# Kernel tuning notes

Measured on AMD Instinct MI355X. Metric: run time of the kernel, lower is better.

The kernel has to match this reference:

```python
import jax, jax.numpy as jnp
import numpy as np


def setup_inputs() -> dict:
    key = jax.random.key(0)
    kx, ks = jax.random.split(key)
    M, N, D = 8192, 8192, 512
    X = jax.random.normal(kx, (M, D), dtype=jnp.float32)
    svs = jax.random.normal(ks, (N, D), dtype=jnp.float32)
    # scale = 1/(2*sigma^2); a plausible fitted value for standard-normal data
    scale = jnp.asarray(0.01, dtype=jnp.float32)
    return {"X": X, "svs": svs, "scale": scale}


def reference(X, svs, scale):
    N, D = svs.shape
    x2 = jnp.sum(X * X, axis=-1, keepdims=True)          # [M, 1]
    s2 = jnp.sum(svs * svs, axis=-1)                      # [N]
    dist2 = x2 + s2[None, :] - 2.0 * (X @ svs.T)          # [M, N]
    dist2 = jnp.maximum(dist2, 0.0)
    log_p = (jax.scipy.special.logsumexp(-scale * dist2, axis=-1)
             - jnp.log(jnp.asarray(N, dtype=X.dtype))
             + (D / 2) * jnp.log(scale / jnp.pi))
    return log_p
```

## Files before the change

kernel.cpp:

```cpp
#include <hip/hip_runtime.h>
#include <hip/hip_bf16.h>
#include <hip/hip_fp8.h>
#include <math.h>

typedef __attribute__((ext_vector_type(4))) int   int4v;
typedef __attribute__((ext_vector_type(8))) int   int8v;
typedef __attribute__((ext_vector_type(4))) float f32x4;

#define BM 128
#define BN 128
#define BK 128

union frag_u { int8v v; int4v h[2]; };

__global__ __launch_bounds__(256) void prep_kernel(
    const float* __restrict__ X, const float* __restrict__ S,
    unsigned char* __restrict__ Xq, unsigned char* __restrict__ Sq,
    float* __restrict__ x2, float* __restrict__ s2,
    float* __restrict__ rowsum, int M, int R, int Dv)
{
    const int gid  = blockIdx.x * 256 + threadIdx.x;
    const int nthr = gridDim.x * 256;

    for (int i = gid; i < M; i += nthr) rowsum[i] = 0.f;

    const int lane = threadIdx.x & 63;
    const int wid  = gid >> 6;
    const int nw   = nthr >> 6;

    for (int row = wid; row < R; row += nw) {
        const float* rp;
        unsigned char* op;
        float* sq;
        if (row < M) { rp = X + (size_t)row * Dv;       op = Xq + (size_t)row * Dv;       sq = x2 + row; }
        else         { rp = S + (size_t)(row - M) * Dv; op = Sq + (size_t)(row - M) * Dv; sq = s2 + (row - M); }

        float acc = 0.f;
        for (int k = lane * 8; k < Dv; k += 64 * 8) {
            float4 v0 = *(const float4*)(rp + k);
            float4 v1 = *(const float4*)(rp + k + 4);
            acc += v0.x * v0.x + v0.y * v0.y + v0.z * v0.z + v0.w * v0.w;
            acc += v1.x * v1.x + v1.y * v1.y + v1.z * v1.z + v1.w * v1.w;
            int lo = __builtin_amdgcn_cvt_pk_fp8_f32(v0.x, v0.y, 0, false);
            lo     = __builtin_amdgcn_cvt_pk_fp8_f32(v0.z, v0.w, lo, true);
            int hi = __builtin_amdgcn_cvt_pk_fp8_f32(v1.x, v1.y, 0, false);
            hi     = __builtin_amdgcn_cvt_pk_fp8_f32(v1.z, v1.w, hi, true);
            union { int i2[2]; uint2 u; } pk;
            pk.i2[0] = lo; pk.i2[1] = hi;
            *(uint2*)(op + k) = pk.u;
        }
#pragma unroll
        for (int off = 1; off < 64; off <<= 1)
            acc += __shfl_xor(acc, off, 64);
        if (lane == 0) *sq = acc;
    }
}

template<int DVC>
__global__ __launch_bounds__(256, 3) void kde_gemm_kernel(
    const unsigned char* __restrict__ Xq,
    const unsigned char* __restrict__ Sq,
    const float* __restrict__ x2,
    const float* __restrict__ s2,
    const float* __restrict__ scale_p,
    float* __restrict__ rowsum,
    int M, int N, int Dv)
{
    const int D = DVC ? DVC : Dv;

    __shared__ char smem[32768];
    unsigned char* As = (unsigned char*)smem;
    unsigned char* Bs = (unsigned char*)(smem + 16384);

    const int tid  = threadIdx.x;
    const int wave = tid >> 6;
    const int lane = tid & 63;
    const int quad = lane >> 4;
    const int l16  = lane & 15;

    const int m0 = blockIdx.x * BM;
    const int n0 = blockIdx.y * BN;
    const int wm = (wave & 1) * 64;
    const int wn = (wave >> 1) * 64;

    const float sc = *scale_p;

    f32x4 acc[4][4] = {};

    const int srow0 = wave * 8 + (lane >> 3);
    const int cg    = (lane & 7) ^ (lane >> 3);
    const unsigned char* gA = Xq + (size_t)(m0 + srow0) * D + cg * 16;
    const unsigned char* gB = Sq + (size_t)(n0 + srow0) * D + cg * 16;

    const int e     = l16 & 7;
    const int offLo = ((2 * quad)     ^ e) * 16;
    const int offHi = ((2 * quad + 1) ^ e) * 16;
    int aOff[4], bOff[4];
#pragma unroll
    for (int i = 0; i < 4; ++i) {
        aOff[i] = (wm + i * 16 + l16) * 128;
        bOff[i] = 16384 + (wn + i * 16 + l16) * 128;
    }

#pragma unroll
    for (int k0 = 0; k0 < D; k0 += BK) {
        __syncthreads();
#pragma unroll
        for (int rd = 0; rd < 4; ++rd)
            __builtin_amdgcn_global_load_lds(
                (const __attribute__((address_space(1))) void*)(gA + (size_t)rd * 32 * D + k0),
                (__attribute__((address_space(3))) void*)(smem + rd * 4096 + wave * 1024),
                16, 0, 0);
#pragma unroll
        for (int rd = 0; rd < 4; ++rd)
            __builtin_amdgcn_global_load_lds(
                (const __attribute__((address_space(1))) void*)(gB + (size_t)rd * 32 * D + k0),
                (__attribute__((address_space(3))) void*)(smem + 16384 + rd * 4096 + wave * 1024),
                16, 0, 0);
        __syncthreads();

        frag_u a_frag[4], b_frag[4];
#pragma unroll
        for (int mi = 0; mi < 4; ++mi) {
            a_frag[mi].h[0] = *(const int4v*)(smem + aOff[mi] + offLo);
            a_frag[mi].h[1] = *(const int4v*)(smem + aOff[mi] + offHi);
        }
#pragma unroll
        for (int ni = 0; ni < 4; ++ni) {
            b_frag[ni].h[0] = *(const int4v*)(smem + bOff[ni] + offLo);
            b_frag[ni].h[1] = *(const int4v*)(smem + bOff[ni] + offHi);
        }
#pragma unroll
        for (int mi = 0; mi < 4; ++mi)
#pragma unroll
            for (int ni = 0; ni < 4; ++ni)
                acc[mi][ni] = __builtin_amdgcn_mfma_scale_f32_16x16x128_f8f6f4(
                    a_frag[mi].v, b_frag[ni].v, acc[mi][ni],
                    0, 0,
                    0, 0x7F7F7F7F,
                    0, 0x7F7F7F7F);
    }

    __syncthreads();
    float* wred = (float*)smem + wave * (64 * 20);

    float s2v[4];
#pragma unroll
    for (int ni = 0; ni < 4; ++ni)
        s2v[ni] = s2[n0 + wn + ni * 16 + l16];

#pragma unroll
    for (int mi = 0; mi < 4; ++mi) {
#pragma unroll
        for (int r = 0; r < 4; ++r) {
            const int rowL = mi * 16 + quad * 4 + r;
            const float xv = x2[m0 + wm + rowL];
            float sum = 0.f;
#pragma unroll
            for (int ni = 0; ni < 4; ++ni) {
                float d2 = xv + s2v[ni] - 2.0f * acc[mi][ni][r];
                d2 = fmaxf(d2, 0.f);
                sum += __expf(-sc * d2);
            }
            wred[rowL * 20 + l16] = sum;
        }
    }
    __syncthreads();

    float4 p0 = *(float4*)(wred + lane * 20 + 0);
    float4 p1 = *(float4*)(wred + lane * 20 + 4);
    float4 p2 = *(float4*)(wred + lane * 20 + 8);
    float4 p3 = *(float4*)(wred + lane * 20 + 12);
    float s = (p0.x + p0.y + p0.z + p0.w) + (p1.x + p1.y + p1.z + p1.w)
            + (p2.x + p2.y + p2.z + p2.w) + (p3.x + p3.y + p3.z + p3.w);
    atomicAdd(&rowsum[m0 + wm + lane], s);
}

__global__ void finalize_kernel(const float* __restrict__ rowsum,
                                const float* __restrict__ scale_p,
                                float* __restrict__ out, int M, int N, int Dv) {
    const int m = blockIdx.x * 256 + threadIdx.x;
    if (m < M) {
        const float sc = *scale_p;
        const float cst = -logf((float)N) + 0.5f * (float)Dv * logf(sc / 3.14159265358979f);
        out[m] = logf(rowsum[m]) + cst;
    }
}

extern "C" void kernel_launch(void* const* d_in, const int* in_sizes, int n_in,
                              void* d_out, int out_size, void* d_ws, size_t ws_size,
                              hipStream_t stream) {
    const float* X       = (const float*)d_in[0];
    const float* S       = (const float*)d_in[1];
    const float* scale_p = (const float*)d_in[2];
    float* out = (float*)d_out;

    const int M  = out_size;
    const int Dv = in_sizes[0] / M;
    const int N  = in_sizes[1] / Dv;

    char* ws = (char*)d_ws;
    unsigned char* Xq = (unsigned char*)ws;
    unsigned char* Sq = (unsigned char*)(ws + (size_t)M * Dv);
    float* x2     = (float*)(ws + (size_t)M * Dv + (size_t)N * Dv);
    float* s2     = x2 + M;
    float* rowsum = s2 + N;

    prep_kernel<<<2048, 256, 0, stream>>>(X, S, Xq, Sq, x2, s2, rowsum, M, M + N, Dv);

    dim3 grid(M / BM, N / BN);
    if (Dv == 512)
        kde_gemm_kernel<512><<<grid, 256, 0, stream>>>(Xq, Sq, x2, s2, scale_p, rowsum, M, N, Dv);
    else
        kde_gemm_kernel<0><<<grid, 256, 0, stream>>>(Xq, Sq, x2, s2, scale_p, rowsum, M, N, Dv);

    finalize_kernel<<<(M + 255) / 256, 256, 0, stream>>>(rowsum, scale_p, out, M, N, Dv);
}
```

Before: 119.6 us.

## Use two waves per block with 64x128 warp tiles in FP8 KDE GEMM

The 128x128 block tile is now computed by 2 waves instead of 4. Each wave owns a 64x128 sub-tile with 4x8 MFMA accumulators. B fragments are loaded in two groups of four so each A fragment feeds more MFMAs, cutting LDS fragment reads per MFMA. The global-to-LDS copy and launch bounds are adjusted for 128 threads. The cost is more accumulator registers per wave and fewer waves per block to hide load and exp latency.

```diff
diff --git a/kernel.cpp b/kernel.cpp
--- a/kernel.cpp
+++ b/kernel.cpp
@@ -57,7 +57,7 @@
 }
 
 template<int DVC>
-__global__ __launch_bounds__(256, 3) void kde_gemm_kernel(
+__global__ __launch_bounds__(128, 2) void kde_gemm_kernel(
     const unsigned char* __restrict__ Xq,
     const unsigned char* __restrict__ Sq,
     const float* __restrict__ x2,
@@ -69,8 +69,6 @@
     const int D = DVC ? DVC : Dv;
 
     __shared__ char smem[32768];
-    unsigned char* As = (unsigned char*)smem;
-    unsigned char* Bs = (unsigned char*)(smem + 16384);
 
     const int tid  = threadIdx.x;
     const int wave = tid >> 6;
@@ -80,74 +78,78 @@
 
     const int m0 = blockIdx.x * BM;
     const int n0 = blockIdx.y * BN;
-    const int wm = (wave & 1) * 64;
-    const int wn = (wave >> 1) * 64;
+    const int wm = wave * 64;
 
     const float sc = *scale_p;
 
-    f32x4 acc[4][4] = {};
-
-    const int srow0 = wave * 8 + (lane >> 3);
-    const int cg    = (lane & 7) ^ (lane >> 3);
+    f32x4 acc[4][8] = {};
+
+    const int srow0 = tid >> 3;
+    const int cg    = (tid & 7) ^ ((tid >> 3) & 7);
     const unsigned char* gA = Xq + (size_t)(m0 + srow0) * D + cg * 16;
     const unsigned char* gB = Sq + (size_t)(n0 + srow0) * D + cg * 16;
 
     const int e     = l16 & 7;
     const int offLo = ((2 * quad)     ^ e) * 16;
     const int offHi = ((2 * quad + 1) ^ e) * 16;
-    int aOff[4], bOff[4];
-#pragma unroll
-    for (int i = 0; i < 4; ++i) {
+    int aOff[4], bOff[8];
+#pragma unroll
+    for (int i = 0; i < 4; ++i)
         aOff[i] = (wm + i * 16 + l16) * 128;
-        bOff[i] = 16384 + (wn + i * 16 + l16) * 128;
-    }
+#pragma unroll
+    for (int i = 0; i < 8; ++i)
+        bOff[i] = 16384 + (i * 16 + l16) * 128;
 
 #pragma unroll
     for (int k0 = 0; k0 < D; k0 += BK) {
         __syncthreads();
 #pragma unroll
-        for (int rd = 0; rd < 4; ++rd)
+        for (int rd = 0; rd < 8; ++rd)
             __builtin_amdgcn_global_load_lds(
-                (const __attribute__((address_space(1))) void*)(gA + (size_t)rd * 32 * D + k0),
-                (__attribute__((address_space(3))) void*)(smem + rd * 4096 + wave * 1024),
+                (const __attribute__((address_space(1))) void*)(gA + (size_t)rd * 16 * D + k0),
+                (__attribute__((address_space(3))) void*)(smem + rd * 2048 + tid * 16),
                 16, 0, 0);
 #pragma unroll
-        for (int rd = 0; rd < 4; ++rd)
+        for (int rd = 0; rd < 8; ++rd)
             __builtin_amdgcn_global_load_lds(
-                (const __attribute__((address_space(1))) void*)(gB + (size_t)rd * 32 * D + k0),
-                (__attribute__((address_space(3))) void*)(smem + 16384 + rd * 4096 + wave * 1024),
+                (const __attribute__((address_space(1))) void*)(gB + (size_t)rd * 16 * D + k0),
+                (__attribute__((address_space(3))) void*)(smem + 16384 + rd * 2048 + tid * 16),
                 16, 0, 0);
         __syncthreads();
 
-        frag_u a_frag[4], b_frag[4];
+        frag_u a_frag[4];
 #pragma unroll
         for (int mi = 0; mi < 4; ++mi) {
             a_frag[mi].h[0] = *(const int4v*)(smem + aOff[mi] + offLo);
             a_frag[mi].h[1] = *(const int4v*)(smem + aOff[mi] + offHi);
         }
 #pragma unroll
-        for (int ni = 0; ni < 4; ++ni) {
-            b_frag[ni].h[0] = *(const int4v*)(smem + bOff[ni] + offLo);
-            b_frag[ni].h[1] = *(const int4v*)(smem + bOff[ni] + offHi);
-        }
-#pragma unroll
-        for (int mi = 0; mi < 4; ++mi)
-#pragma unroll
-            for (int ni = 0; ni < 4; ++ni)
-                acc[mi][ni] = __builtin_amdgcn_mfma_scale_f32_16x16x128_f8f6f4(
-                    a_frag[mi].v, b_frag[ni].v, acc[mi][ni],
-                    0, 0,
-                    0, 0x7F7F7F7F,
-                    0, 0x7F7F7F7F);
+        for (int g = 0; g < 2; ++g) {
+            frag_u b_frag[4];
+#pragma unroll
+            for (int nj = 0; nj < 4; ++nj) {
+                b_frag[nj].h[0] = *(const int4v*)(smem + bOff[g * 4 + nj] + offLo);
+                b_frag[nj].h[1] = *(const int4v*)(smem + bOff[g * 4 + nj] + offHi);
+            }
+#pragma unroll
+            for (int mi = 0; mi < 4; ++mi)
+#pragma unroll
+                for (int nj = 0; nj < 4; ++nj)
+                    acc[mi][g * 4 + nj] = __builtin_amdgcn_mfma_scale_f32_16x16x128_f8f6f4(
+                        a_frag[mi].v, b_frag[nj].v, acc[mi][g * 4 + nj],
+                        0, 0,
+                        0, 0x7F7F7F7F,
+                        0, 0x7F7F7F7F);
+        }
     }
 
     __syncthreads();
     float* wred = (float*)smem + wave * (64 * 20);
 
-    float s2v[4];
-#pragma unroll
-    for (int ni = 0; ni < 4; ++ni)
-        s2v[ni] = s2[n0 + wn + ni * 16 + l16];
+    float s2v[8];
+#pragma unroll
+    for (int ni = 0; ni < 8; ++ni)
+        s2v[ni] = s2[n0 + ni * 16 + l16];
 
 #pragma unroll
     for (int mi = 0; mi < 4; ++mi) {
@@ -157,7 +159,7 @@
             const float xv = x2[m0 + wm + rowL];
             float sum = 0.f;
 #pragma unroll
-            for (int ni = 0; ni < 4; ++ni) {
+            for (int ni = 0; ni < 8; ++ni) {
                 float d2 = xv + s2v[ni] - 2.0f * acc[mi][ni][r];
                 d2 = fmaxf(d2, 0.f);
                 sum += __expf(-sc * d2);
@@ -210,9 +212,9 @@
 
     dim3 grid(M / BM, N / BN);
     if (Dv == 512)
-        kde_gemm_kernel<512><<<grid, 256, 0, stream>>>(Xq, Sq, x2, s2, scale_p, rowsum, M, N, Dv);
+        kde_gemm_kernel<512><<<grid, 128, 0, stream>>>(Xq, Sq, x2, s2, scale_p, rowsum, M, N, Dv);
     else
-        kde_gemm_kernel<0><<<grid, 256, 0, stream>>>(Xq, Sq, x2, s2, scale_p, rowsum, M, N, Dv);
+        kde_gemm_kernel<0><<<grid, 128, 0, stream>>>(Xq, Sq, x2, s2, scale_p, rowsum, M, N, Dv);
 
     finalize_kernel<<<(M + 255) / 256, 256, 0, stream>>>(rowsum, scale_p, out, M, N, Dv);
 }
```

Result: slower. 122.9 us (+2.7%).
